# Kernel tuning notes

Hardware: AMD Instinct MI355X
Metric: run time of the kernel (lower is better)

The kernel has to match this reference:

```python
import jax, jax.numpy as jnp
import numpy as np

NUM_FIELDS = 24
FIELD_DIM = 2000
VOCAB = NUM_FIELDS * FIELD_DIM  # sum(field_dims) = 48000
EMBED_DIM = 64
H1, H2 = 64, 32
NUM_INTERACTIONS = 16
BATCH = 4096


def setup_inputs() -> dict:
    key = jax.random.key(0)
    ks = jax.random.split(key, 12)
    s = 0.05  # xavier-ish scale
    return {
        "x": jax.random.randint(ks[0], (BATCH, NUM_FIELDS), 0, FIELD_DIM, dtype=jnp.int32),
        # per-field embedding tables stacked: (num_fields, vocab, embed_dim)
        "tables": jax.random.normal(ks[1], (NUM_FIELDS, VOCAB, EMBED_DIM), jnp.float32) * s,
        "fc_w": jax.random.normal(ks[2], (VOCAB, 1), jnp.float32) * s,
        "fc_b": jnp.zeros((1,), jnp.float32),
        "w1": jax.random.normal(ks[3], (2 * EMBED_DIM, H1), jnp.float32) * s,
        "b1": jnp.zeros((H1,), jnp.float32),
        "w2": jax.random.normal(ks[4], (H1, H2), jnp.float32) * s,
        "b2": jnp.zeros((H2,), jnp.float32),
        "w3": jax.random.normal(ks[5], (H2, 1), jnp.float32) * s,
        "b3": jnp.zeros((1,), jnp.float32),
        "proj_w": jax.random.normal(ks[6], (EMBED_DIM, 1), jnp.float32) * s,
        "proj_b": jnp.zeros((1,), jnp.float32),
        "bias": jnp.zeros((1,), jnp.float32),
    }


def reference(x, tables, fc_w, fc_b, w1, b1, w2, b2, w3, b3, proj_w, proj_b, bias):
    offsets = jnp.arange(NUM_FIELDS, dtype=x.dtype) * FIELD_DIM  # cumsum of equal field_dims
    idx = x + offsets[None, :]  # (B, F)

    # FeaturesLinear: first-order term, (B, 1)
    linear_part = fc_w[idx].sum(axis=1) + fc_b

    # FeaturesEmbedding: per-field table lookup -> (B, F, D)
    emb = tables[jnp.arange(NUM_FIELDS)[None, :], idx]

    # FeatureInteractionDetector: all i<j pairs, concat, score with MLP
    iu, ju = jnp.triu_indices(NUM_FIELDS, k=1)  # (P,), P = F*(F-1)/2
    pair_emb = jnp.concatenate([emb[:, iu], emb[:, ju]], axis=-1)  # (B, P, 2D)
    h = jax.nn.relu(pair_emb @ w1 + b1)
    h = jax.nn.relu(h @ w2 + b2)
    scores = (h @ w3 + b3)[..., 0]  # (B, P)

    # topk over batch-mean scores, gather per-sample scores and pair indices
    _, top = jax.lax.top_k(scores.mean(axis=0), NUM_INTERACTIONS)  # (K,)
    sel_scores = scores[:, top]  # (B, K)
    sel_i, sel_j = iu[top], ju[top]

    # FeatureCrossing: elementwise product of selected pairs, score-weighted sum, project
    crossed = emb[:, sel_i] * emb[:, sel_j]  # (B, K, D)
    summed = jnp.sum(crossed * sel_scores[..., None], axis=1)  # (B, D)
    crossed_part = summed @ proj_w + proj_b  # (B, 1)

    out = linear_part + crossed_part + bias  # (B, 1)
    return out[:, 0]
```

## Files before the change

kernel.cpp:

```cpp
#include <hip/hip_runtime.h>
#include <stdint.h>

#define NF 24
#define FD 2000
#define VOCABSZ 48000
#define ED 64
#define H1D 64
#define H2D 32
#define NPAIR 276
#define BATCH 4096
#define NSEL 16
#define NTILE 256
#define PBASE 49152

typedef _Float16 f16x8 __attribute__((ext_vector_type(8)));
typedef float f32x4 __attribute__((ext_vector_type(4)));

union U4 { f16x8 v; uint32_t u[4]; uint4 q; };

__device__ __forceinline__ uint32_t pkrtz(float lo, float hi){
  uint32_t r; asm("v_cvt_pkrtz_f16_f32 %0, %1, %2" : "=v"(r) : "v"(lo), "v"(hi)); return r;
}
__device__ __forceinline__ uint32_t pk_add(uint32_t a, uint32_t b){
  uint32_t r; asm("v_pk_add_f16 %0, %1, %2" : "=v"(r) : "v"(a), "v"(b)); return r;
}
__device__ __forceinline__ uint32_t pk_relu(uint32_t a){
  uint32_t r; asm("v_pk_max_f16 %0, %1, %2" : "=v"(r) : "v"(a), "v"(0u)); return r;
}

__global__ __launch_bounds__(1024) void k_pair(
    const int* __restrict__ x, const float* __restrict__ tables,
    const float* __restrict__ w1, const float* __restrict__ b1,
    const float* __restrict__ w2, const float* __restrict__ b2,
    const float* __restrict__ w3, const float* __restrict__ b3,
    float* __restrict__ scores, float* __restrict__ part){
  __shared__ __align__(16) char smem[147456];
  const int tid  = threadIdx.x;
  const int bt   = blockIdx.x;
  const int lane = tid & 63;
  const int w    = tid >> 6;
  const int n    = lane & 15;
  const int kg   = lane >> 4;

  const int half = w >> 3;
  const int oq   = (w >> 1) & 3;
  const int fg   = w & 1;
  const int isPt = (half == 0);
  const float b3v = b3[0];

  const int o = 16*oq + n;
  U4 wp0, wp1;
  {
    const float* wsrc = w1 + (size_t)(isPt ? 0 : ED)*H1D + o;
    #pragma unroll
    for(int j=0;j<8;j++) wp0.v[j] = (_Float16)wsrc[(kg*8+j)*H1D];
    #pragma unroll
    for(int j=0;j<8;j++) wp1.v[j] = (_Float16)wsrc[(32+kg*8+j)*H1D];
  }
  const float b1v = isPt ? b1[o] : 0.f;

  U4 wf[2][2];
  #pragma unroll
  for(int kh=0;kh<2;kh++)
    #pragma unroll
    for(int nh=0;nh<2;nh++)
      #pragma unroll
      for(int q2=0;q2<4;q2++){
        float lo = w2[(kg*8 + 2*q2     + 32*kh)*H2D + n + 16*nh];
        float hi = w2[(kg*8 + 2*q2 + 1 + 32*kh)*H2D + n + 16*nh];
        wf[kh][nh].u[q2] = pkrtz(lo, hi);
      }
  const float b2v0 = b2[n], b2v1 = b2[n+16];
  const float w3v0 = w3[n], w3v1 = w3[n+16];

  #pragma unroll
  for(int i=0;i<3;i++){
    int c = i*1024 + tid;
    int rid = c >> 3;
    int qc = c & 7;
    int f = rid >> 4, b = rid & 15;
    int xv = x[(bt*16 + b)*NF + f];
    const float4* rp = (const float4*)(tables + ((size_t)f*VOCABSZ + (size_t)f*FD + (size_t)xv)*ED + qc*8);
    float4 v0 = rp[0], v1 = rp[1];
    uint4 pk;
    pk.x = pkrtz(v0.x, v0.y); pk.y = pkrtz(v0.z, v0.w);
    pk.z = pkrtz(v1.x, v1.y); pk.w = pkrtz(v1.z, v1.w);
    uint32_t db = ((uint32_t)(f*2048 + b*128 + qc*16)) ^ ((uint32_t)(b&7)<<4);
    *(uint4*)(smem + db) = pk;
  }
  __syncthreads();

  {
    const uint32_t rswz = ((uint32_t)(n&7))<<4;
    const int slab0 = isPt ? 0 : 24;
    for(int ff=0; ff<12; ff++){
      int f = fg*12 + ff;
      U4 a0, a1;
      a0.q = *(const uint4*)(smem + (((uint32_t)(f*2048 + n*128      + kg*16)) ^ rswz));
      a1.q = *(const uint4*)(smem + (((uint32_t)(f*2048 + n*128 + 64 + kg*16)) ^ rswz));
      f32x4 acc = {b1v, b1v, b1v, b1v};
      acc = __builtin_amdgcn_mfma_f32_16x16x32_f16(a0.v, wp0.v, acc, 0,0,0);
      acc = __builtin_amdgcn_mfma_f32_16x16x32_f16(a1.v, wp1.v, acc, 0,0,0);
      int sl = slab0 + f;
      #pragma unroll
      for(int r=0;r<4;r++){
        float up = __shfl_xor(acc[r], 1, 64);
        if((lane & 1) == 0){
          int bo = kg*4 + r;
          int k2 = 8*oq + (n>>1);
          uint32_t db = ((uint32_t)(PBASE + sl*2048 + bo*128 + k2*4)) ^ ((uint32_t)(bo&7)<<4);
          *(uint32_t*)(smem + db) = pkrtz(acc[r], up);
        }
      }
    }
  }
  __syncthreads();

  {
    int p0, np;
    if(w < 4){ np = 18; p0 = w*18; } else { np = 17; p0 = 72 + (w-4)*17; }
    int ii = 0, rem = p0;
    while(rem >= (NF-1-ii)){ rem -= (NF-1-ii); ii++; }
    int jj = ii + 1 + rem;

    const uint32_t aswz = ((uint32_t)(n&7))<<4;
    const uint32_t rowoff = (uint32_t)n*128;
    const uint32_t qoff = (uint32_t)kg*16;

    for(int t=0;t<np;t++){
      int p = p0 + t;
      uint32_t tb = (uint32_t)(PBASE + ii*2048) + rowoff;
      uint32_t ub = (uint32_t)(PBASE + (24+jj)*2048) + rowoff;
      uint4 a0 = *(const uint4*)(smem + ((tb + qoff     ) ^ aswz));
      uint4 a1 = *(const uint4*)(smem + ((tb + qoff + 64 ) ^ aswz));
      uint4 c0 = *(const uint4*)(smem + ((ub + qoff     ) ^ aswz));
      uint4 c1 = *(const uint4*)(smem + ((ub + qoff + 64 ) ^ aswz));

      U4 h0, h1;
      h0.u[0]=pk_relu(pk_add(a0.x,c0.x)); h0.u[1]=pk_relu(pk_add(a0.y,c0.y));
      h0.u[2]=pk_relu(pk_add(a0.z,c0.z)); h0.u[3]=pk_relu(pk_add(a0.w,c0.w));
      h1.u[0]=pk_relu(pk_add(a1.x,c1.x)); h1.u[1]=pk_relu(pk_add(a1.y,c1.y));
      h1.u[2]=pk_relu(pk_add(a1.z,c1.z)); h1.u[3]=pk_relu(pk_add(a1.w,c1.w));

      f32x4 acc0 = {0.f,0.f,0.f,0.f}, acc1 = {0.f,0.f,0.f,0.f};
      acc0 = __builtin_amdgcn_mfma_f32_16x16x32_f16(h0.v, wf[0][0].v, acc0, 0,0,0);
      acc0 = __builtin_amdgcn_mfma_f32_16x16x32_f16(h1.v, wf[1][0].v, acc0, 0,0,0);
      acc1 = __builtin_amdgcn_mfma_f32_16x16x32_f16(h0.v, wf[0][1].v, acc1, 0,0,0);
      acc1 = __builtin_amdgcn_mfma_f32_16x16x32_f16(h1.v, wf[1][1].v, acc1, 0,0,0);

      float vsum[4];
      #pragma unroll
      for(int r=0;r<4;r++){
        float v0 = acc0[r] + b2v0; v0 = v0>0.f?v0:0.f;
        float v1 = acc1[r] + b2v1; v1 = v1>0.f?v1:0.f;
        float s = v0*w3v0 + v1*w3v1;
        #pragma unroll
        for(int m=1;m<16;m<<=1) s += __shfl_xor(s, m, 64);
        vsum[r] = s;
      }
      if(n == 0){
        float* sp = scores + (size_t)p*BATCH + bt*16 + kg*4;
        sp[0]=vsum[0]+b3v; sp[1]=vsum[1]+b3v; sp[2]=vsum[2]+b3v; sp[3]=vsum[3]+b3v;
      }
      float ps = vsum[0]+vsum[1]+vsum[2]+vsum[3];
      ps += __shfl_xor(ps, 16, 64);
      ps += __shfl_xor(ps, 32, 64);
      if(lane == 0) part[(size_t)p*NTILE + bt] = ps + 16.f*b3v;
      if(++jj == NF){ ii++; jj = ii+1; }
    }
  }
}

__global__ __launch_bounds__(1024) void k_final(
    const int* __restrict__ x, const float* __restrict__ tables,
    const float* __restrict__ scores, const float* __restrict__ part,
    const float* __restrict__ fc_w, const float* __restrict__ fc_b,
    const float* __restrict__ proj_w, const float* __restrict__ proj_b,
    const float* __restrict__ bias, float* __restrict__ out){
  __shared__ float means[NPAIR];
  __shared__ int sel[NSEL];
  __shared__ unsigned short pairIJ[NPAIR];
  int tid = threadIdx.x;
  int bt = blockIdx.x;

  if(tid < NPAIR){
    int ii=0, rem=tid;
    while(rem >= NF-1-ii){ rem -= NF-1-ii; ii++; }
    pairIJ[tid] = (unsigned short)((ii<<8) | (ii+1+rem));
    const float4* pp = (const float4*)(part + (size_t)tid*NTILE);
    float4 s4 = {0.f,0.f,0.f,0.f};
    #pragma unroll 8
    for(int i=0;i<NTILE/4;i++){
      float4 v = pp[i];
      s4.x += v.x; s4.y += v.y; s4.z += v.z; s4.w += v.w;
    }
    means[tid] = (s4.x + s4.y) + (s4.z + s4.w);
  }
  __syncthreads();
  if(tid < 64){
    int l = tid;
    float v[5];
    #pragma unroll
    for(int q=0;q<5;q++){
      int i = l + q*64;
      v[q] = (i < NPAIR) ? means[i] : -3.0e38f;
    }
    for(int s=0;s<NSEL;s++){
      float bv = v[0]; int bslot = 0;
      #pragma unroll
      for(int q=1;q<5;q++){ if(v[q] > bv){ bv = v[q]; bslot = q; } }
      int bi = l + bslot*64;
      float cv = bv; int ci = bi;
      #pragma unroll
      for(int m=1;m<64;m<<=1){
        float ov = __shfl_xor(cv, m, 64);
        int   oi = __shfl_xor(ci, m, 64);
        if(ov > cv || (ov == cv && oi < ci)){ cv = ov; ci = oi; }
      }
      if(l == 0) sel[s] = ci;
      if(bi == ci) v[bslot] = -3.0e38f;
    }
  }
  __syncthreads();

  int row = tid >> 6, lane = tid & 63;
  int brow = bt*16 + row;
  float acc = 0.f;
  #pragma unroll
  for(int t=0;t<NSEL;t++){
    int p = sel[t];
    int ij = pairIJ[p];
    int ii = ij >> 8, jj = ij & 255;
    int xi = x[brow*NF+ii], xj = x[brow*NF+jj];
    float ei = tables[((size_t)ii*VOCABSZ + (size_t)ii*FD + (size_t)xi)*ED + lane];
    float ej = tables[((size_t)jj*VOCABSZ + (size_t)jj*FD + (size_t)xj)*ED + lane];
    float s = scores[(size_t)p*BATCH + brow];
    acc += ei*ej*s;
  }
  float v = acc * proj_w[lane];
  if(lane < NF) v += fc_w[x[brow*NF+lane] + lane*FD];
  #pragma unroll
  for(int m=1;m<64;m<<=1) v += __shfl_xor(v, m, 64);
  if(lane == 0) out[brow] = v + fc_b[0] + proj_b[0] + bias[0];
}

extern "C" void kernel_launch(void* const* d_in, const int* in_sizes, int n_in,
                              void* d_out, int out_size, void* d_ws, size_t ws_size,
                              hipStream_t stream){
  const int*   x      = (const int*)  d_in[0];
  const float* tables = (const float*)d_in[1];
  const float* fc_w   = (const float*)d_in[2];
  const float* fc_b   = (const float*)d_in[3];
  const float* w1     = (const float*)d_in[4];
  const float* b1     = (const float*)d_in[5];
  const float* w2     = (const float*)d_in[6];
  const float* b2     = (const float*)d_in[7];
  const float* w3     = (const float*)d_in[8];
  const float* b3     = (const float*)d_in[9];
  const float* proj_w = (const float*)d_in[10];
  const float* proj_b = (const float*)d_in[11];
  const float* bias   = (const float*)d_in[12];
  float* out = (float*)d_out;

  float* scores = (float*)d_ws;
  float* part   = scores + (size_t)NPAIR*BATCH;

  k_pair<<<NTILE, 1024, 0, stream>>>(x, tables, w1, b1, w2, b2, w3, b3, scores, part);
  k_final<<<NTILE, 1024, 0, stream>>>(x, tables, scores, part, fc_w, fc_b, proj_w, proj_b, bias, out);
}
```

Baseline: 56.35 us.

## Precompute per-pair projected cross term in pair kernel, simplify final kernel

The pair kernel now also computes, for every pair and sample, the dot product of the elementwise embedding product with proj_w, multiplies it by the score, and stores that scalar. The final kernel then only sums 16 selected scalars plus the linear term, with no second gather of embedding rows from the large tables. This removes scattered global gathers in the final kernel. In exchange it adds packed-f16 multiplies, a projection and shuffles for all 276 pairs, and the cross product is now computed in fp16 instead of fp32. It also caches the i-row loads across iterations.

Result: no change. 56.65 us (+0.5%).

```diff
diff --git a/kernel.cpp b/kernel.cpp
--- a/kernel.cpp
+++ b/kernel.cpp
@@ -24,6 +24,9 @@
 __device__ __forceinline__ uint32_t pk_add(uint32_t a, uint32_t b){
   uint32_t r; asm("v_pk_add_f16 %0, %1, %2" : "=v"(r) : "v"(a), "v"(b)); return r;
 }
+__device__ __forceinline__ uint32_t pk_mul(uint32_t a, uint32_t b){
+  uint32_t r; asm("v_pk_mul_f16 %0, %1, %2" : "=v"(r) : "v"(a), "v"(b)); return r;
+}
 __device__ __forceinline__ uint32_t pk_relu(uint32_t a){
   uint32_t r; asm("v_pk_max_f16 %0, %1, %2" : "=v"(r) : "v"(a), "v"(0u)); return r;
 }
@@ -33,7 +36,8 @@
     const float* __restrict__ w1, const float* __restrict__ b1,
     const float* __restrict__ w2, const float* __restrict__ b2,
     const float* __restrict__ w3, const float* __restrict__ b3,
-    float* __restrict__ scores, float* __restrict__ part){
+    const float* __restrict__ proj_w,
+    float* __restrict__ sgarr, float* __restrict__ part){
   __shared__ __align__(16) char smem[147456];
   const int tid  = threadIdx.x;
   const int bt   = blockIdx.x;
@@ -72,6 +76,10 @@
       }
   const float b2v0 = b2[n], b2v1 = b2[n+16];
   const float w3v0 = w3[n], w3v1 = w3[n+16];
+
+  float pwr[16];
+  #pragma unroll
+  for(int q=0;q<16;q++) pwr[q] = proj_w[kg*16 + q];
 
   #pragma unroll
   for(int i=0;i<3;i++){
@@ -126,27 +134,50 @@
     const uint32_t aswz = ((uint32_t)(n&7))<<4;
     const uint32_t rowoff = (uint32_t)n*128;
     const uint32_t qoff = (uint32_t)kg*16;
+    const uint32_t kg32 = (uint32_t)kg*32;
+
+    int cached_i = -1;
+    U4 ta0, ta1, ei0, ei1;
 
     for(int t=0;t<np;t++){
       int p = p0 + t;
-      uint32_t tb = (uint32_t)(PBASE + ii*2048) + rowoff;
+      if(ii != cached_i){
+        uint32_t tb = (uint32_t)(PBASE + ii*2048) + rowoff;
+        ta0.q = *(const uint4*)(smem + ((tb + qoff     ) ^ aswz));
+        ta1.q = *(const uint4*)(smem + ((tb + qoff + 64) ^ aswz));
+        uint32_t ebi = (uint32_t)(ii*2048) + rowoff + kg32;
+        ei0.q = *(const uint4*)(smem + ((ebi     ) ^ aswz));
+        ei1.q = *(const uint4*)(smem + ((ebi + 16) ^ aswz));
+        cached_i = ii;
+      }
       uint32_t ub = (uint32_t)(PBASE + (24+jj)*2048) + rowoff;
-      uint4 a0 = *(const uint4*)(smem + ((tb + qoff     ) ^ aswz));
-      uint4 a1 = *(const uint4*)(smem + ((tb + qoff + 64 ) ^ aswz));
       uint4 c0 = *(const uint4*)(smem + ((ub + qoff     ) ^ aswz));
-      uint4 c1 = *(const uint4*)(smem + ((ub + qoff + 64 ) ^ aswz));
+      uint4 c1 = *(const uint4*)(smem + ((ub + qoff + 64) ^ aswz));
+      uint32_t ebj = (uint32_t)(jj*2048) + rowoff + kg32;
+      U4 ej0, ej1;
+      ej0.q = *(const uint4*)(smem + ((ebj     ) ^ aswz));
+      ej1.q = *(const uint4*)(smem + ((ebj + 16) ^ aswz));
 
       U4 h0, h1;
-      h0.u[0]=pk_relu(pk_add(a0.x,c0.x)); h0.u[1]=pk_relu(pk_add(a0.y,c0.y));
-      h0.u[2]=pk_relu(pk_add(a0.z,c0.z)); h0.u[3]=pk_relu(pk_add(a0.w,c0.w));
-      h1.u[0]=pk_relu(pk_add(a1.x,c1.x)); h1.u[1]=pk_relu(pk_add(a1.y,c1.y));
-      h1.u[2]=pk_relu(pk_add(a1.z,c1.z)); h1.u[3]=pk_relu(pk_add(a1.w,c1.w));
+      h0.u[0]=pk_relu(pk_add(ta0.u[0],c0.x)); h0.u[1]=pk_relu(pk_add(ta0.u[1],c0.y));
+      h0.u[2]=pk_relu(pk_add(ta0.u[2],c0.z)); h0.u[3]=pk_relu(pk_add(ta0.u[3],c0.w));
+      h1.u[0]=pk_relu(pk_add(ta1.u[0],c1.x)); h1.u[1]=pk_relu(pk_add(ta1.u[1],c1.y));
+      h1.u[2]=pk_relu(pk_add(ta1.u[2],c1.z)); h1.u[3]=pk_relu(pk_add(ta1.u[3],c1.w));
 
       f32x4 acc0 = {0.f,0.f,0.f,0.f}, acc1 = {0.f,0.f,0.f,0.f};
       acc0 = __builtin_amdgcn_mfma_f32_16x16x32_f16(h0.v, wf[0][0].v, acc0, 0,0,0);
       acc0 = __builtin_amdgcn_mfma_f32_16x16x32_f16(h1.v, wf[1][0].v, acc0, 0,0,0);
       acc1 = __builtin_amdgcn_mfma_f32_16x16x32_f16(h0.v, wf[0][1].v, acc1, 0,0,0);
       acc1 = __builtin_amdgcn_mfma_f32_16x16x32_f16(h1.v, wf[1][1].v, acc1, 0,0,0);
+
+      U4 m0, m1;
+      #pragma unroll
+      for(int q=0;q<4;q++){ m0.u[q] = pk_mul(ei0.u[q], ej0.u[q]); m1.u[q] = pk_mul(ei1.u[q], ej1.u[q]); }
+      float gp = 0.f;
+      #pragma unroll
+      for(int j=0;j<8;j++) gp += (float)m0.v[j]*pwr[j] + (float)m1.v[j]*pwr[8+j];
+      gp += __shfl_xor(gp, 16, 64);
+      gp += __shfl_xor(gp, 32, 64);
 
       float vsum[4];
       #pragma unroll
@@ -158,35 +189,38 @@
         for(int m=1;m<16;m<<=1) s += __shfl_xor(s, m, 64);
         vsum[r] = s;
       }
-      if(n == 0){
-        float* sp = scores + (size_t)p*BATCH + bt*16 + kg*4;
-        sp[0]=vsum[0]+b3v; sp[1]=vsum[1]+b3v; sp[2]=vsum[2]+b3v; sp[3]=vsum[3]+b3v;
-      }
+
+      int rs = n & 3;
+      float v_sel = vsum[0];
+      v_sel = (rs==1) ? vsum[1] : v_sel;
+      v_sel = (rs==2) ? vsum[2] : v_sel;
+      v_sel = (rs==3) ? vsum[3] : v_sel;
+      float sc_n = __shfl(v_sel, ((n>>2)<<4) | (n&3), 64) + b3v;
+
+      if(lane < 16) sgarr[(size_t)p*BATCH + bt*16 + lane] = sc_n * gp;
+
       float ps = vsum[0]+vsum[1]+vsum[2]+vsum[3];
       ps += __shfl_xor(ps, 16, 64);
       ps += __shfl_xor(ps, 32, 64);
       if(lane == 0) part[(size_t)p*NTILE + bt] = ps + 16.f*b3v;
+
       if(++jj == NF){ ii++; jj = ii+1; }
     }
   }
 }
 
 __global__ __launch_bounds__(1024) void k_final(
-    const int* __restrict__ x, const float* __restrict__ tables,
-    const float* __restrict__ scores, const float* __restrict__ part,
+    const int* __restrict__ x, const float* __restrict__ sgarr,
+    const float* __restrict__ part,
     const float* __restrict__ fc_w, const float* __restrict__ fc_b,
-    const float* __restrict__ proj_w, const float* __restrict__ proj_b,
-    const float* __restrict__ bias, float* __restrict__ out){
+    const float* __restrict__ proj_b, const float* __restrict__ bias,
+    float* __restrict__ out){
   __shared__ float means[NPAIR];
   __shared__ int sel[NSEL];
-  __shared__ unsigned short pairIJ[NPAIR];
   int tid = threadIdx.x;
   int bt = blockIdx.x;
 
   if(tid < NPAIR){
-    int ii=0, rem=tid;
-    while(rem >= NF-1-ii){ rem -= NF-1-ii; ii++; }
-    pairIJ[tid] = (unsigned short)((ii<<8) | (ii+1+rem));
     const float4* pp = (const float4*)(part + (size_t)tid*NTILE);
     float4 s4 = {0.f,0.f,0.f,0.f};
     #pragma unroll 8
@@ -225,20 +259,13 @@
 
   int row = tid >> 6, lane = tid & 63;
   int brow = bt*16 + row;
-  float acc = 0.f;
-  #pragma unroll
-  for(int t=0;t<NSEL;t++){
-    int p = sel[t];
-    int ij = pairIJ[p];
-    int ii = ij >> 8, jj = ij & 255;
-    int xi = x[brow*NF+ii], xj = x[brow*NF+jj];
-    float ei = tables[((size_t)ii*VOCABSZ + (size_t)ii*FD + (size_t)xi)*ED + lane];
-    float ej = tables[((size_t)jj*VOCABSZ + (size_t)jj*FD + (size_t)xj)*ED + lane];
-    float s = scores[(size_t)p*BATCH + brow];
-    acc += ei*ej*s;
-  }
-  float v = acc * proj_w[lane];
-  if(lane < NF) v += fc_w[x[brow*NF+lane] + lane*FD];
+  float v = 0.f;
+  if(lane < NSEL){
+    v = sgarr[(size_t)sel[lane]*BATCH + brow];
+  } else if(lane >= 32 && lane < 32+NF){
+    int fl = lane - 32;
+    v = fc_w[x[brow*NF + fl] + fl*FD];
+  }
   #pragma unroll
   for(int m=1;m<64;m<<=1) v += __shfl_xor(v, m, 64);
   if(lane == 0) out[brow] = v + fc_b[0] + proj_b[0] + bias[0];
@@ -262,9 +289,9 @@
   const float* bias   = (const float*)d_in[12];
   float* out = (float*)d_out;
 
-  float* scores = (float*)d_ws;
-  float* part   = scores + (size_t)NPAIR*BATCH;
-
-  k_pair<<<NTILE, 1024, 0, stream>>>(x, tables, w1, b1, w2, b2, w3, b3, scores, part);
-  k_final<<<NTILE, 1024, 0, stream>>>(x, tables, scores, part, fc_w, fc_b, proj_w, proj_b, bias, out);
-}
+  float* sgarr = (float*)d_ws;
+  float* part  = sgarr + (size_t)NPAIR*BATCH;
+
+  k_pair<<<NTILE, 1024, 0, stream>>>(x, tables, w1, b1, w2, b2, w3, b3, proj_w, sgarr, part);
+  k_final<<<NTILE, 1024, 0, stream>>>(x, sgarr, part, fc_w, fc_b, proj_b, bias, out);
+}
```
